# Optimization experiments

Hardware: AMD Instinct MI355X
Metric: run time of the kernel (lower is better)

## Reference

```python
import jax, jax.numpy as jnp
import numpy as np

N = 10000   # num_nodes
E = 320000  # num_edges (avg degree 32)
IN, HID, OUT = 512, 512, 256


def setup_inputs() -> dict:
    key = jax.random.key(0)
    ks = jax.random.split(key, 19)
    rn = lambda k, shape: (jax.random.normal(k, shape, jnp.float32) * 0.05)
    edge_index = jax.random.randint(ks[0], (2, E), 0, N, dtype=jnp.int32)
    return {
        "edge_index": edge_index,
        "w_pe": rn(ks[1], (IN, N)), "b_pe": rn(ks[2], (IN,)),
        "w_self0": rn(ks[3], (HID, IN)), "w_neigh0": rn(ks[4], (HID, IN)), "b0": rn(ks[5], (HID,)),
        "w_res0": rn(ks[6], (HID, IN)), "rb0": rn(ks[7], (HID,)),
        "w_self1": rn(ks[8], (HID, HID)), "w_neigh1": rn(ks[9], (HID, HID)), "b1": rn(ks[10], (HID,)),
        "w_res1": rn(ks[11], (HID, HID)), "rb1": rn(ks[12], (HID,)),
        "w_self2": rn(ks[13], (OUT, HID)), "w_neigh2": rn(ks[14], (OUT, HID)), "b2": rn(ks[15], (OUT,)),
        "w_res2": rn(ks[16], (OUT, HID)), "rb2": rn(ks[17], (OUT,)),
    }


def reference(edge_index, w_pe, b_pe,
              w_self0, w_neigh0, b0, w_res0, rb0,
              w_self1, w_neigh1, b1, w_res1, rb1,
              w_self2, w_neigh2, b2, w_res2, rb2):
    src, dst = edge_index[0], edge_index[1]

    def mean_agg(h):
        # mean of neighbor features per destination node (sparse SAGE aggregation)
        s = jax.ops.segment_sum(h[src], dst, num_segments=N)           # [N, D]
        deg = jax.ops.segment_sum(jnp.ones((E,), h.dtype), dst, num_segments=N)
        return s / jnp.maximum(deg, 1.0)[:, None]

    # pe = Linear(eye(N)) as in the original module
    pe = jnp.eye(N, dtype=w_pe.dtype) @ w_pe.T + b_pe                   # [N, IN]

    layers = [
        (w_self0, w_neigh0, b0, w_res0, rb0),
        (w_self1, w_neigh1, b1, w_res1, rb1),
        (w_self2, w_neigh2, b2, w_res2, rb2),
    ]

    h = pe
    mids = []
    for i, (ws, wn, b, wr, rb) in enumerate(layers):
        h_prev = h
        # SAGEConv (mean): fc_self(h) + fc_neigh(mean_neigh(h))
        h = h @ ws.T + mean_agg(h_prev) @ wn.T + b
        if i != len(layers) - 1:
            h = jax.nn.leaky_relu(h, 0.01)
            # F.dropout with training=False is identity (inference reference)
        h = h + (h_prev @ wr.T + rb)  # residual linear
        mids.append(h)
    return (h, *mids)
```

## Files before the change

### kernel.cpp

```cpp
#include <hip/hip_runtime.h>

#define N_NODES 10000
#define N_EDGES 320000
#define DIN 512
#define DHID 512
#define DOUT 256

typedef __bf16 bf16x8 __attribute__((ext_vector_type(8)));
typedef float f32x4 __attribute__((ext_vector_type(4)));
typedef unsigned short ushort_t;
typedef unsigned int uint_t;

__device__ __forceinline__ float b2f(ushort_t u){
    union { uint_t i; float f; } v; v.i = (uint_t)u << 16; return v.f;
}
__device__ __forceinline__ float blo(uint_t v){
    union { uint_t i; float f; } u; u.i = v << 16; return u.f;
}
__device__ __forceinline__ float bhi(uint_t v){
    union { uint_t i; float f; } u; u.i = v & 0xffff0000u; return u.f;
}
__device__ __forceinline__ ushort_t f2b(float f){
    union { float f; uint_t i; } v; v.f = f;
    uint_t i = v.i;
    return (ushort_t)((i + 0x7fffu + ((i >> 16) & 1u)) >> 16);
}

__device__ __forceinline__ void gll16(const ushort_t* g, ushort_t* l){
    __builtin_amdgcn_global_load_lds(
        (const __attribute__((address_space(1))) unsigned int*)g,
        (__attribute__((address_space(3))) unsigned int*)l,
        16, 0, 0);
}


__global__ void k_zero(int* __restrict__ deg, uint_t* __restrict__ zp){
    int i = blockIdx.x * 256 + threadIdx.x;
    if (i < N_NODES) deg[i] = 0;
    if (i < 256) zp[i] = 0u;
}

__global__ void k_degree(const int* __restrict__ dst, int* __restrict__ deg){
    int e = blockIdx.x * 256 + threadIdx.x;
    if (e < N_EDGES) atomicAdd(&deg[dst[e]], 1);
}

__global__ void k_scan(const int* __restrict__ deg, int* __restrict__ row_ptr,
                       int* __restrict__ cursor){
    __shared__ int part[256];
    int t = threadIdx.x;
    int base = t * 40;
    int loc[40];
    int s = 0;
    #pragma unroll
    for (int i = 0; i < 40; ++i){
        int idx = base + i;
        int v = (idx < N_NODES) ? deg[idx] : 0;
        s += v; loc[i] = s;
    }
    part[t] = s;
    __syncthreads();
    int val = s;
    for (int off = 1; off < 256; off <<= 1){
        int x = (t >= off) ? part[t - off] : 0;
        __syncthreads();
        val += x; part[t] = val;
        __syncthreads();
    }
    int exc = val - s;
    if (t == 0) row_ptr[0] = 0;
    int run = exc;
    #pragma unroll
    for (int i = 0; i < 40; ++i){
        int idx = base + i;
        if (idx < N_NODES){
            row_ptr[idx + 1] = exc + loc[i];
            cursor[idx] = run;
        }
        run = exc + loc[i];
    }
}

__global__ void k_scatter(const int* __restrict__ src, const int* __restrict__ dst,
                          int* __restrict__ cursor, int* __restrict__ srcs){
    int e = blockIdx.x * 256 + threadIdx.x;
    if (e < N_EDGES){
        int p = atomicAdd(&cursor[dst[e]], 1);
        srcs[p] = src[e];
    }
}


struct CvtArgs { const float* s[8]; const float* s2[8]; ushort_t* d[8]; int n[8]; };

__global__ void k_cvt(CvtArgs a){
    int m = blockIdx.y;
    int i = (blockIdx.x * 256 + threadIdx.x) * 8;
    if (i < a.n[m]){
        const float* sp = a.s[m] + i;
        float4 f0 = *(const float4*)sp;
        float4 f1 = *(const float4*)(sp + 4);
        if (a.s2[m]){
            const float* sq = a.s2[m] + i;
            float4 g0 = *(const float4*)sq;
            float4 g1 = *(const float4*)(sq + 4);
            f0.x += g0.x; f0.y += g0.y; f0.z += g0.z; f0.w += g0.w;
            f1.x += g1.x; f1.y += g1.y; f1.z += g1.z; f1.w += g1.w;
        }
        uint4 u;
        u.x = (uint_t)f2b(f0.x) | ((uint_t)f2b(f0.y) << 16);
        u.y = (uint_t)f2b(f0.z) | ((uint_t)f2b(f0.w) << 16);
        u.z = (uint_t)f2b(f1.x) | ((uint_t)f2b(f1.y) << 16);
        u.w = (uint_t)f2b(f1.z) | ((uint_t)f2b(f1.w) << 16);
        *(uint4*)&a.d[m][i] = u;
    }
}


__global__ void k_pe(const float* __restrict__ w_pe, const float* __restrict__ b_pe,
                     ushort_t* __restrict__ h0){
    __shared__ float lt[64][68];
    int t = threadIdx.x;
    int n0 = blockIdx.x * 64, i0 = blockIdx.y * 64;
    int nc = (t & 15) * 4, ir = t >> 4;
    #pragma unroll
    for (int p = 0; p < 4; ++p){
        int i_loc = ir + p * 16;
        float4 v = {0.f, 0.f, 0.f, 0.f};
        if (n0 + nc < N_NODES)
            v = *(const float4*)&w_pe[(size_t)(i0 + i_loc) * N_NODES + n0 + nc];
        lt[nc + 0][i_loc] = v.x;
        lt[nc + 1][i_loc] = v.y;
        lt[nc + 2][i_loc] = v.z;
        lt[nc + 3][i_loc] = v.w;
    }
    __syncthreads();
    int ic = t & 7, nr = t >> 3;
    #pragma unroll
    for (int p = 0; p < 2; ++p){
        int n_loc = nr + p * 32;
        int n = n0 + n_loc;
        if (n < N_NODES){
            uint4 u;
            uint_t w01 = (uint_t)f2b(lt[n_loc][ic*8+0] + b_pe[i0+ic*8+0])
                       | ((uint_t)f2b(lt[n_loc][ic*8+1] + b_pe[i0+ic*8+1]) << 16);
            uint_t w23 = (uint_t)f2b(lt[n_loc][ic*8+2] + b_pe[i0+ic*8+2])
                       | ((uint_t)f2b(lt[n_loc][ic*8+3] + b_pe[i0+ic*8+3]) << 16);
            uint_t w45 = (uint_t)f2b(lt[n_loc][ic*8+4] + b_pe[i0+ic*8+4])
                       | ((uint_t)f2b(lt[n_loc][ic*8+5] + b_pe[i0+ic*8+5]) << 16);
            uint_t w67 = (uint_t)f2b(lt[n_loc][ic*8+6] + b_pe[i0+ic*8+6])
                       | ((uint_t)f2b(lt[n_loc][ic*8+7] + b_pe[i0+ic*8+7]) << 16);
            u.x = w01; u.y = w23; u.z = w45; u.w = w67;
            *(uint4*)&h0[(size_t)n * DIN + i0 + ic * 8] = u;
        }
    }
}


#define AGG_EDGE(e, CH) { \
    int s_ = __builtin_amdgcn_readlane(sr, (e)); \
    uint_t v_ = *(const uint_t*)&X[((size_t)(uint_t)s_ << 9) + col]; \
    CH##0 += blo(v_); CH##1 += bhi(v_); }

__global__ __launch_bounds__(256) void k_agg(
    const ushort_t* __restrict__ X, const int* __restrict__ row_ptr,
    const int* __restrict__ srcs, ushort_t* __restrict__ out, int dummy)
{
    int w = threadIdx.x >> 6, lane = threadIdx.x & 63;
    int n = blockIdx.x * 4 + w;
    int col = blockIdx.y * 128 + lane * 2;
    int beg = row_ptr[n], end = row_ptr[n + 1];
    int deg = end - beg;
    float a0=0.f,a1=0.f, p0=0.f,p1=0.f, c0=0.f,c1=0.f, d0=0.f,d1=0.f;

    for (int base = beg; base < end; base += 64){
        int rem = end - base;
        int sr = (lane < rem) ? srcs[base + lane] : dummy;
        int cnt = rem < 64 ? rem : 64;
        #pragma unroll
        for (int k = 0; k < 4; ++k){
            if (k * 16 < cnt){
                int L = k * 16;
                AGG_EDGE(L + 0,  a) AGG_EDGE(L + 1,  p) AGG_EDGE(L + 2,  c) AGG_EDGE(L + 3,  d)
                AGG_EDGE(L + 4,  a) AGG_EDGE(L + 5,  p) AGG_EDGE(L + 6,  c) AGG_EDGE(L + 7,  d)
                AGG_EDGE(L + 8,  a) AGG_EDGE(L + 9,  p) AGG_EDGE(L + 10, c) AGG_EDGE(L + 11, d)
                AGG_EDGE(L + 12, a) AGG_EDGE(L + 13, p) AGG_EDGE(L + 14, c) AGG_EDGE(L + 15, d)
            }
        }
    }

    float r0 = (a0 + p0) + (c0 + d0);
    float r1 = (a1 + p1) + (c1 + d1);
    float inv = (deg > 0) ? 1.f / (float)deg : 1.f;
    uint_t o = (uint_t)f2b(r0 * inv) | ((uint_t)f2b(r1 * inv) << 16);
    *(uint_t*)&out[(size_t)n * 512 + col] = o;
}


#define AGGF_EDGE(e, CH) { \
    int s_ = __builtin_amdgcn_readlane(sr, (e)); \
    uint_t v_ = *(const uint_t*)&P[((size_t)(uint_t)s_ << 8) + col]; \
    CH##0 += blo(v_); CH##1 += bhi(v_); }

__global__ __launch_bounds__(256) void k_aggf(
    const ushort_t* __restrict__ P, const int* __restrict__ row_ptr,
    const int* __restrict__ srcs, const float* __restrict__ Q,
    float* __restrict__ fin, float* __restrict__ mid2, int dummy)
{
    int w = threadIdx.x >> 6, lane = threadIdx.x & 63;
    int n = blockIdx.x * 4 + w;
    int col = blockIdx.y * 128 + lane * 2;
    int beg = row_ptr[n], end = row_ptr[n + 1];
    int deg = end - beg;
    float a0=0.f,a1=0.f, p0=0.f,p1=0.f, c0=0.f,c1=0.f, d0=0.f,d1=0.f;

    for (int base = beg; base < end; base += 64){
        int rem = end - base;
        int sr = (lane < rem) ? srcs[base + lane] : dummy;
        int cnt = rem < 64 ? rem : 64;
        #pragma unroll
        for (int k = 0; k < 4; ++k){
            if (k * 16 < cnt){
                int L = k * 16;
                AGGF_EDGE(L + 0,  a) AGGF_EDGE(L + 1,  p) AGGF_EDGE(L + 2,  c) AGGF_EDGE(L + 3,  d)
                AGGF_EDGE(L + 4,  a) AGGF_EDGE(L + 5,  p) AGGF_EDGE(L + 6,  c) AGGF_EDGE(L + 7,  d)
                AGGF_EDGE(L + 8,  a) AGGF_EDGE(L + 9,  p) AGGF_EDGE(L + 10, c) AGGF_EDGE(L + 11, d)
                AGGF_EDGE(L + 12, a) AGGF_EDGE(L + 13, p) AGGF_EDGE(L + 14, c) AGGF_EDGE(L + 15, d)
            }
        }
    }

    float r0 = (a0 + p0) + (c0 + d0);
    float r1 = (a1 + p1) + (c1 + d1);
    float inv = (deg > 0) ? 1.f / (float)deg : 1.f;
    float2 q = *(const float2*)&Q[(size_t)n * 256 + col];
    float2 o;
    o.x = q.x + r0 * inv;
    o.y = q.y + r1 * inv;
    *(float2*)&fin [(size_t)n * 256 + col] = o;
    *(float2*)&mid2[(size_t)n * 256 + col] = o;
}


template<int DO, int BN, bool ACT, bool WRITE_BF>
__global__ __launch_bounds__(256, 2) void k_layer(
    const ushort_t* __restrict__ X, const ushort_t* __restrict__ G,
    const ushort_t* __restrict__ Ws, const ushort_t* __restrict__ Wn,
    const ushort_t* __restrict__ Wr,
    const float* __restrict__ b, const float* __restrict__ rb,
    float* __restrict__ Y, ushort_t* __restrict__ YB)
{
    constexpr int BM   = 160;
    constexpr int NT   = DO / BN;
    constexpr int WTN  = BN / 32;
    constexpr int NCH  = (2 * BM + 3 * BN) / 16;
    constexpr int CHPW = (NCH + 3) / 4;
    constexpr int OG   = BM * 32;
    constexpr int OS   = 2 * BM * 32;
    constexpr int WS32 = BN * 32;
    constexpr int BUFSZ = OS + 3 * WS32;
    __shared__ __align__(16) ushort_t smem[2][BUFSZ];

    int t = threadIdx.x;
    int bid = blockIdx.x;
    int r8 = bid & 7, q8 = bid >> 3;
    int m_t = (q8 / NT) * 8 + r8;
    int n_t = q8 % NT;
    if (m_t * BM >= N_NODES) return;
    int m0 = m_t * BM, n0 = n_t * BN;

    int lane = t & 63, w = t >> 6;
    int wr = w >> 1, wc = w & 1;

    const ushort_t* gptr[CHPW];
    int coff[CHPW];
    bool gv[CHPW];
    int rl = lane >> 2, sl = (lane & 3) * 8;
    #pragma unroll
    for (int i = 0; i < CHPW; ++i){
        int qq = w * CHPW + i;
        gv[i] = (qq < NCH);
        int qc = gv[i] ? qq : 0;
        const ushort_t* gA; int rowbase, off;
        if (qc < 10)      { gA = X;  rowbase = m0 + qc * 16;        off = qc * 512; }
        else if (qc < 20) { gA = G;  rowbase = m0 + (qc - 10) * 16; off = OG + (qc - 10) * 512; }
        else {
            int q2 = qc - 20;
            int sec = q2 / (BN / 16), wi = q2 % (BN / 16);
            gA = (sec == 0) ? Ws : (sec == 1) ? Wn : Wr;
            rowbase = n0 + wi * 16;
            off = OS + sec * WS32 + wi * 512;
        }
        gptr[i] = gA + (size_t)(rowbase + rl) * 512 + sl;
        coff[i] = off;
    }

    f32x4 accS[5][WTN] = {}, accG[5][WTN] = {}, accR[5][WTN] = {};
    int r16 = lane & 15;
    int arow = wr * 80 + r16;
    int brow = wc * (BN / 2) + r16;
    int kk = (lane >> 4) * 8;

    #pragma unroll
    for (int i = 0; i < CHPW; ++i) if (gv[i]) gll16(gptr[i], &smem[0][coff[i]]);
    __syncthreads();

    int cur = 0;
    for (int ks = 0; ks < 16; ++ks){
        if (ks < 15){
            int k0 = (ks + 1) * 32;
            #pragma unroll
            for (int i = 0; i < CHPW; ++i) if (gv[i]) gll16(gptr[i] + k0, &smem[cur ^ 1][coff[i]]);
        }

        const ushort_t* sb = smem[cur];
        bf16x8 ax[5], ag[5], bs[WTN], bn_[WTN], brr[WTN];
        #pragma unroll
        for (int m = 0; m < 5; ++m){
            ax[m] = *(const bf16x8*)&sb[(arow + m * 16) * 32 + kk];
            ag[m] = *(const bf16x8*)&sb[OG + (arow + m * 16) * 32 + kk];
        }
        #pragma unroll
        for (int n = 0; n < WTN; ++n){
            bs[n]  = *(const bf16x8*)&sb[OS            + (brow + n * 16) * 32 + kk];
            bn_[n] = *(const bf16x8*)&sb[OS + WS32     + (brow + n * 16) * 32 + kk];
            brr[n] = *(const bf16x8*)&sb[OS + 2 * WS32 + (brow + n * 16) * 32 + kk];
        }
        #pragma unroll
        for (int m = 0; m < 5; ++m)
            #pragma unroll
            for (int n = 0; n < WTN; ++n){
                accS[m][n] = __builtin_amdgcn_mfma_f32_16x16x32_bf16(ax[m], bs[n],  accS[m][n], 0, 0, 0);
                accG[m][n] = __builtin_amdgcn_mfma_f32_16x16x32_bf16(ag[m], bn_[n], accG[m][n], 0, 0, 0);
                accR[m][n] = __builtin_amdgcn_mfma_f32_16x16x32_bf16(ax[m], brr[n], accR[m][n], 0, 0, 0);
            }

        __syncthreads();
        cur ^= 1;
    }

    int col_l = lane & 15;
    int row_l = (lane >> 4) * 4;
    #pragma unroll
    for (int n = 0; n < WTN; ++n){
        int col = n0 + wc * (BN / 2) + n * 16 + col_l;
        float bb = b[col], rbb = rb[col];
        #pragma unroll
        for (int m = 0; m < 5; ++m){
            #pragma unroll
            for (int j = 0; j < 4; ++j){
                int row = m0 + wr * 80 + m * 16 + row_l + j;
                if (row < N_NODES){
                    float v = accS[m][n][j] + accG[m][n][j] + bb;
                    if (ACT) v = (v > 0.f) ? v : 0.01f * v;
                    v += accR[m][n][j] + rbb;
                    Y[(size_t)row * DO + col] = v;
                    if (WRITE_BF) YB[(size_t)row * DO + col] = f2b(v);
                }
            }
        }
    }
}


__global__ __launch_bounds__(256, 2) void k_layer2(
    const ushort_t* __restrict__ X,
    const ushort_t* __restrict__ Wn, const ushort_t* __restrict__ Wsr,
    const float* __restrict__ b, const float* __restrict__ rb,
    ushort_t* __restrict__ Pout, float* __restrict__ Qout)
{
    constexpr int BM = 160, BN = 32, NT = DOUT / BN;
    constexpr int NCH = 10 + 2 * (BN / 16);
    constexpr int CHPW = 4;
    constexpr int OWN = BM * 32;
    constexpr int OWS = OWN + BN * 32;
    constexpr int BUFSZ = OWS + BN * 32;
    __shared__ __align__(16) ushort_t smem[2][BUFSZ];

    int t = threadIdx.x;
    int bid = blockIdx.x;
    int r8 = bid & 7, q8 = bid >> 3;
    int m_t = (q8 / NT) * 8 + r8;
    int n_t = q8 % NT;
    if (m_t * BM >= N_NODES) return;
    int m0 = m_t * BM, n0 = n_t * BN;

    int lane = t & 63, w = t >> 6;
    int wr = w >> 1, wc = w & 1;

    const ushort_t* gptr[CHPW];
    int coff[CHPW];
    bool gv[CHPW];
    int rl = lane >> 2, sl = (lane & 3) * 8;
    #pragma unroll
    for (int i = 0; i < CHPW; ++i){
        int qq = w * CHPW + i;
        gv[i] = (qq < NCH);
        int qc = gv[i] ? qq : 0;
        const ushort_t* gA; int rowbase, off;
        if (qc < 10)      { gA = X;   rowbase = m0 + qc * 16;        off = qc * 512; }
        else if (qc < 12) { gA = Wn;  rowbase = n0 + (qc - 10) * 16; off = OWN + (qc - 10) * 512; }
        else              { gA = Wsr; rowbase = n0 + (qc - 12) * 16; off = OWS + (qc - 12) * 512; }
        gptr[i] = gA + (size_t)(rowbase + rl) * 512 + sl;
        coff[i] = off;
    }

    f32x4 accP[5] = {}, accQ[5] = {};
    int r16 = lane & 15;
    int arow = wr * 80 + r16;
    int brow = wc * 16 + r16;
    int kk = (lane >> 4) * 8;

    #pragma unroll
    for (int i = 0; i < CHPW; ++i) if (gv[i]) gll16(gptr[i], &smem[0][coff[i]]);
    __syncthreads();

    int cur = 0;
    for (int ks = 0; ks < 16; ++ks){
        if (ks < 15){
            int k0 = (ks + 1) * 32;
            #pragma unroll
            for (int i = 0; i < CHPW; ++i) if (gv[i]) gll16(gptr[i] + k0, &smem[cur ^ 1][coff[i]]);
        }

        const ushort_t* sb = smem[cur];
        bf16x8 ax[5];
        #pragma unroll
        for (int m = 0; m < 5; ++m)
            ax[m] = *(const bf16x8*)&sb[(arow + m * 16) * 32 + kk];
        bf16x8 bn_ = *(const bf16x8*)&sb[OWN + brow * 32 + kk];
        bf16x8 bsr = *(const bf16x8*)&sb[OWS + brow * 32 + kk];
        #pragma unroll
        for (int m = 0; m < 5; ++m){
            accP[m] = __builtin_amdgcn_mfma_f32_16x16x32_bf16(ax[m], bn_, accP[m], 0, 0, 0);
            accQ[m] = __builtin_amdgcn_mfma_f32_16x16x32_bf16(ax[m], bsr, accQ[m], 0, 0, 0);
        }

        __syncthreads();
        cur ^= 1;
    }

    int col_l = lane & 15;
    int row_l = (lane >> 4) * 4;
    int col = n0 + wc * 16 + col_l;
    float bb = b[col] + rb[col];
    #pragma unroll
    for (int m = 0; m < 5; ++m){
        #pragma unroll
        for (int j = 0; j < 4; ++j){
            int row = m0 + wr * 80 + m * 16 + row_l + j;
            if (row < N_NODES){
                Qout[(size_t)row * DOUT + col] = accQ[m][j] + bb;
                Pout[(size_t)row * DOUT + col] = f2b(accP[m][j]);
            }
        }
    }
}


extern "C" void kernel_launch(void* const* d_in, const int* in_sizes, int n_in,
                              void* d_out, int out_size, void* d_ws, size_t ws_size,
                              hipStream_t stream) {
    const int* edge  = (const int*)d_in[0];
    const int* e_src = edge;
    const int* e_dst = edge + N_EDGES;
    const float* w_pe = (const float*)d_in[1];
    const float* b_pe = (const float*)d_in[2];
    const float* ws0 = (const float*)d_in[3];
    const float* wn0 = (const float*)d_in[4];
    const float* b0  = (const float*)d_in[5];
    const float* wr0 = (const float*)d_in[6];
    const float* rb0 = (const float*)d_in[7];
    const float* ws1 = (const float*)d_in[8];
    const float* wn1 = (const float*)d_in[9];
    const float* b1  = (const float*)d_in[10];
    const float* wr1 = (const float*)d_in[11];
    const float* rb1 = (const float*)d_in[12];
    const float* ws2 = (const float*)d_in[13];
    const float* wn2 = (const float*)d_in[14];
    const float* b2  = (const float*)d_in[15];
    const float* wr2 = (const float*)d_in[16];
    const float* rb2 = (const float*)d_in[17];

    char* wsb = (char*)d_ws;
    ushort_t* h0   = (ushort_t*)wsb;
    ushort_t* hb   = (ushort_t*)(wsb + 10240000);
    ushort_t* aggb = (ushort_t*)(wsb + 20480000);
    ushort_t* wbf  = (ushort_t*)(wsb + 30720000);
    int* deg     = (int*)(wsb + 34652160);
    int* row_ptr = deg + 10016;
    int* cursor  = row_ptr + 10016;
    int* srcs    = cursor + 10016;
    uint_t* zp   = (uint_t*)(wsb + 36052992);
    const int dummy_h0 = 35208;
    const int dummy_hb = 25208;
    const int dummy_pb = 30416;

    ushort_t* wbf0s = wbf;
    ushort_t* wbf0n = wbf + 262144;
    ushort_t* wbf0r = wbf + 524288;
    ushort_t* wbf1s = wbf + 786432;
    ushort_t* wbf1n = wbf + 1048576;
    ushort_t* wbf1r = wbf + 1310720;
    ushort_t* wbf2n = wbf + 1572864;
    ushort_t* wbf2sr= wbf + 1703936;

    float* out  = (float*)d_out;
    float* fin  = out;
    float* mid0 = out + 2560000;
    float* mid1 = out + 7680000;
    float* mid2 = out + 12800000;
    ushort_t* pb = aggb;

    k_zero   <<<40, 256, 0, stream>>>(deg, zp);
    k_degree <<<1250, 256, 0, stream>>>(e_dst, deg);
    k_scan   <<<1, 256, 0, stream>>>(deg, row_ptr, cursor);
    k_scatter<<<1250, 256, 0, stream>>>(e_src, e_dst, cursor, srcs);

    CvtArgs ca;
    ca.s[0]=ws0; ca.s[1]=wn0; ca.s[2]=wr0;
    ca.s[3]=ws1; ca.s[4]=wn1; ca.s[5]=wr1;
    ca.s[6]=wn2; ca.s[7]=ws2;
    for (int i = 0; i < 8; ++i) ca.s2[i] = nullptr;
    ca.s2[7] = wr2;
    ca.d[0]=wbf0s; ca.d[1]=wbf0n; ca.d[2]=wbf0r;
    ca.d[3]=wbf1s; ca.d[4]=wbf1n; ca.d[5]=wbf1r;
    ca.d[6]=wbf2n; ca.d[7]=wbf2sr;
    for (int i = 0; i < 6; ++i) ca.n[i] = 262144;
    ca.n[6] = 131072; ca.n[7] = 131072;
    k_cvt<<<dim3(128, 8), 256, 0, stream>>>(ca);

    k_pe<<<dim3(157, 8), 256, 0, stream>>>(w_pe, b_pe, h0);

    k_agg<<<dim3(2500, 4), 256, 0, stream>>>(h0, row_ptr, srcs, aggb, dummy_h0);
    k_layer<512, 64, true, true ><<<dim3(512), 256, 0, stream>>>(
        h0, aggb, wbf0s, wbf0n, wbf0r, b0, rb0, mid0, hb);

    k_agg<<<dim3(2500, 4), 256, 0, stream>>>(hb, row_ptr, srcs, aggb, dummy_hb);
    k_layer<512, 64, true, true ><<<dim3(512), 256, 0, stream>>>(
        hb, aggb, wbf1s, wbf1n, wbf1r, b1, rb1, mid1, h0);

    k_layer2<<<dim3(512), 256, 0, stream>>>(h0, wbf2n, wbf2sr, b2, rb2, pb, mid2);
    k_aggf<<<dim3(2500, 2), 256, 0, stream>>>(pb, row_ptr, srcs, mid2, fin, mid2, dummy_pb);
}
```

Baseline: 214.1 us.

## Merge prologue kernels and process two nodes per wave in aggregation

Folds the weight conversion, positional-embedding transpose and degree zeroing into one launch, cutting three kernel launches. The aggregation kernels now assign each half-wave to its own destination node and have each lane load 8-byte uint2 chunks, halving the grid and doubling the bytes per load. The two halves of a wave loop to the larger of their two degrees, so some work is wasted when neighbouring nodes' degrees differ.

```diff
diff --git a/kernel.cpp b/kernel.cpp
--- a/kernel.cpp
+++ b/kernel.cpp
@@ -33,12 +33,6 @@
         16, 0, 0);
 }
 
-
-__global__ void k_zero(int* __restrict__ deg, uint_t* __restrict__ zp){
-    int i = blockIdx.x * 256 + threadIdx.x;
-    if (i < N_NODES) deg[i] = 0;
-    if (i < 256) zp[i] = 0u;
-}
 
 __global__ void k_degree(const int* __restrict__ dst, int* __restrict__ deg){
     int e = blockIdx.x * 256 + threadIdx.x;
@@ -93,114 +87,127 @@
 
 struct CvtArgs { const float* s[8]; const float* s2[8]; ushort_t* d[8]; int n[8]; };
 
-__global__ void k_cvt(CvtArgs a){
-    int m = blockIdx.y;
-    int i = (blockIdx.x * 256 + threadIdx.x) * 8;
-    if (i < a.n[m]){
-        const float* sp = a.s[m] + i;
-        float4 f0 = *(const float4*)sp;
-        float4 f1 = *(const float4*)(sp + 4);
-        if (a.s2[m]){
-            const float* sq = a.s2[m] + i;
-            float4 g0 = *(const float4*)sq;
-            float4 g1 = *(const float4*)(sq + 4);
-            f0.x += g0.x; f0.y += g0.y; f0.z += g0.z; f0.w += g0.w;
-            f1.x += g1.x; f1.y += g1.y; f1.z += g1.z; f1.w += g1.w;
-        }
-        uint4 u;
-        u.x = (uint_t)f2b(f0.x) | ((uint_t)f2b(f0.y) << 16);
-        u.y = (uint_t)f2b(f0.z) | ((uint_t)f2b(f0.w) << 16);
-        u.z = (uint_t)f2b(f1.x) | ((uint_t)f2b(f1.y) << 16);
-        u.w = (uint_t)f2b(f1.z) | ((uint_t)f2b(f1.w) << 16);
-        *(uint4*)&a.d[m][i] = u;
-    }
-}
-
-
-__global__ void k_pe(const float* __restrict__ w_pe, const float* __restrict__ b_pe,
-                     ushort_t* __restrict__ h0){
+__global__ void k_pro(const float* __restrict__ w_pe, const float* __restrict__ b_pe,
+                      ushort_t* __restrict__ h0, CvtArgs a,
+                      int* __restrict__ deg, uint_t* __restrict__ zp){
     __shared__ float lt[64][68];
+    int bid = blockIdx.x;
     int t = threadIdx.x;
-    int n0 = blockIdx.x * 64, i0 = blockIdx.y * 64;
-    int nc = (t & 15) * 4, ir = t >> 4;
-    #pragma unroll
-    for (int p = 0; p < 4; ++p){
-        int i_loc = ir + p * 16;
-        float4 v = {0.f, 0.f, 0.f, 0.f};
-        if (n0 + nc < N_NODES)
-            v = *(const float4*)&w_pe[(size_t)(i0 + i_loc) * N_NODES + n0 + nc];
-        lt[nc + 0][i_loc] = v.x;
-        lt[nc + 1][i_loc] = v.y;
-        lt[nc + 2][i_loc] = v.z;
-        lt[nc + 3][i_loc] = v.w;
-    }
-    __syncthreads();
-    int ic = t & 7, nr = t >> 3;
-    #pragma unroll
-    for (int p = 0; p < 2; ++p){
-        int n_loc = nr + p * 32;
-        int n = n0 + n_loc;
-        if (n < N_NODES){
+    if (bid < 1256){
+        int n0 = (bid % 157) * 64, i0 = (bid / 157) * 64;
+        int nc = (t & 15) * 4, ir = t >> 4;
+        #pragma unroll
+        for (int p = 0; p < 4; ++p){
+            int i_loc = ir + p * 16;
+            float4 v = {0.f, 0.f, 0.f, 0.f};
+            if (n0 + nc < N_NODES)
+                v = *(const float4*)&w_pe[(size_t)(i0 + i_loc) * N_NODES + n0 + nc];
+            lt[nc + 0][i_loc] = v.x;
+            lt[nc + 1][i_loc] = v.y;
+            lt[nc + 2][i_loc] = v.z;
+            lt[nc + 3][i_loc] = v.w;
+        }
+        __syncthreads();
+        int ic = t & 7, nr = t >> 3;
+        #pragma unroll
+        for (int p = 0; p < 2; ++p){
+            int n_loc = nr + p * 32;
+            int n = n0 + n_loc;
+            if (n < N_NODES){
+                uint4 u;
+                u.x = (uint_t)f2b(lt[n_loc][ic*8+0] + b_pe[i0+ic*8+0])
+                    | ((uint_t)f2b(lt[n_loc][ic*8+1] + b_pe[i0+ic*8+1]) << 16);
+                u.y = (uint_t)f2b(lt[n_loc][ic*8+2] + b_pe[i0+ic*8+2])
+                    | ((uint_t)f2b(lt[n_loc][ic*8+3] + b_pe[i0+ic*8+3]) << 16);
+                u.z = (uint_t)f2b(lt[n_loc][ic*8+4] + b_pe[i0+ic*8+4])
+                    | ((uint_t)f2b(lt[n_loc][ic*8+5] + b_pe[i0+ic*8+5]) << 16);
+                u.w = (uint_t)f2b(lt[n_loc][ic*8+6] + b_pe[i0+ic*8+6])
+                    | ((uint_t)f2b(lt[n_loc][ic*8+7] + b_pe[i0+ic*8+7]) << 16);
+                *(uint4*)&h0[(size_t)n * DIN + i0 + ic * 8] = u;
+            }
+        }
+    } else if (bid < 2280){
+        int j = bid - 1256;
+        int m = j >> 7;
+        int i = (((j & 127) * 256) + t) * 8;
+        if (i < a.n[m]){
+            const float* sp = a.s[m] + i;
+            float4 f0 = *(const float4*)sp;
+            float4 f1 = *(const float4*)(sp + 4);
+            if (a.s2[m]){
+                const float* sq = a.s2[m] + i;
+                float4 g0 = *(const float4*)sq;
+                float4 g1 = *(const float4*)(sq + 4);
+                f0.x += g0.x; f0.y += g0.y; f0.z += g0.z; f0.w += g0.w;
+                f1.x += g1.x; f1.y += g1.y; f1.z += g1.z; f1.w += g1.w;
+            }
             uint4 u;
-            uint_t w01 = (uint_t)f2b(lt[n_loc][ic*8+0] + b_pe[i0+ic*8+0])
-                       | ((uint_t)f2b(lt[n_loc][ic*8+1] + b_pe[i0+ic*8+1]) << 16);
-            uint_t w23 = (uint_t)f2b(lt[n_loc][ic*8+2] + b_pe[i0+ic*8+2])
-                       | ((uint_t)f2b(lt[n_loc][ic*8+3] + b_pe[i0+ic*8+3]) << 16);
-            uint_t w45 = (uint_t)f2b(lt[n_loc][ic*8+4] + b_pe[i0+ic*8+4])
-                       | ((uint_t)f2b(lt[n_loc][ic*8+5] + b_pe[i0+ic*8+5]) << 16);
-            uint_t w67 = (uint_t)f2b(lt[n_loc][ic*8+6] + b_pe[i0+ic*8+6])
-                       | ((uint_t)f2b(lt[n_loc][ic*8+7] + b_pe[i0+ic*8+7]) << 16);
-            u.x = w01; u.y = w23; u.z = w45; u.w = w67;
-            *(uint4*)&h0[(size_t)n * DIN + i0 + ic * 8] = u;
-        }
-    }
-}
-
-
-#define AGG_EDGE(e, CH) { \
-    int s_ = __builtin_amdgcn_readlane(sr, (e)); \
-    uint_t v_ = *(const uint_t*)&X[((size_t)(uint_t)s_ << 9) + col]; \
-    CH##0 += blo(v_); CH##1 += bhi(v_); }
+            u.x = (uint_t)f2b(f0.x) | ((uint_t)f2b(f0.y) << 16);
+            u.y = (uint_t)f2b(f0.z) | ((uint_t)f2b(f0.w) << 16);
+            u.z = (uint_t)f2b(f1.x) | ((uint_t)f2b(f1.y) << 16);
+            u.w = (uint_t)f2b(f1.z) | ((uint_t)f2b(f1.w) << 16);
+            *(uint4*)&a.d[m][i] = u;
+        }
+    } else {
+        int i = (bid - 2280) * 256 + t;
+        if (i < N_NODES) deg[i] = 0;
+        if (i < 256) zp[i] = 0u;
+    }
+}
+
+
+#define DUAL_EDGE(X, SH, e, CH) { \
+    int rA_ = __builtin_amdgcn_readlane(sr, (e)); \
+    int rB_ = __builtin_amdgcn_readlane(sr, 32 + (e)); \
+    int row_ = half ? rB_ : rA_; \
+    uint2 v_ = *(const uint2*)&X[((size_t)(uint_t)row_ << SH) + col]; \
+    CH##0 += blo(v_.x); CH##1 += bhi(v_.x); CH##2 += blo(v_.y); CH##3 += bhi(v_.y); }
 
 __global__ __launch_bounds__(256) void k_agg(
     const ushort_t* __restrict__ X, const int* __restrict__ row_ptr,
     const int* __restrict__ srcs, ushort_t* __restrict__ out, int dummy)
 {
     int w = threadIdx.x >> 6, lane = threadIdx.x & 63;
-    int n = blockIdx.x * 4 + w;
-    int col = blockIdx.y * 128 + lane * 2;
+    int half = lane >> 5, l32 = lane & 31;
+    int n = blockIdx.x * 8 + w * 2 + half;
+    int col = blockIdx.y * 128 + l32 * 4;
     int beg = row_ptr[n], end = row_ptr[n + 1];
     int deg = end - beg;
-    float a0=0.f,a1=0.f, p0=0.f,p1=0.f, c0=0.f,c1=0.f, d0=0.f,d1=0.f;
-
-    for (int base = beg; base < end; base += 64){
-        int rem = end - base;
-        int sr = (lane < rem) ? srcs[base + lane] : dummy;
-        int cnt = rem < 64 ? rem : 64;
-        #pragma unroll
-        for (int k = 0; k < 4; ++k){
+    int degMax = max(deg, __shfl_xor(deg, 32));
+    float a0=0.f,a1=0.f,a2=0.f,a3=0.f, b0=0.f,b1=0.f,b2=0.f,b3=0.f;
+    float c0=0.f,c1=0.f,c2=0.f,c3=0.f, d0=0.f,d1=0.f,d2=0.f,d3=0.f;
+
+    for (int base = 0; base < degMax; base += 32){
+        int rem = deg - base;
+        int sr = (l32 < rem) ? srcs[beg + base + l32] : dummy;
+        int cnt = degMax - base; if (cnt > 32) cnt = 32;
+        #pragma unroll
+        for (int k = 0; k < 2; ++k){
             if (k * 16 < cnt){
                 int L = k * 16;
-                AGG_EDGE(L + 0,  a) AGG_EDGE(L + 1,  p) AGG_EDGE(L + 2,  c) AGG_EDGE(L + 3,  d)
-                AGG_EDGE(L + 4,  a) AGG_EDGE(L + 5,  p) AGG_EDGE(L + 6,  c) AGG_EDGE(L + 7,  d)
-                AGG_EDGE(L + 8,  a) AGG_EDGE(L + 9,  p) AGG_EDGE(L + 10, c) AGG_EDGE(L + 11, d)
-                AGG_EDGE(L + 12, a) AGG_EDGE(L + 13, p) AGG_EDGE(L + 14, c) AGG_EDGE(L + 15, d)
-            }
-        }
-    }
-
-    float r0 = (a0 + p0) + (c0 + d0);
-    float r1 = (a1 + p1) + (c1 + d1);
+                DUAL_EDGE(X, 9, L + 0,  a) DUAL_EDGE(X, 9, L + 1,  b)
+                DUAL_EDGE(X, 9, L + 2,  c) DUAL_EDGE(X, 9, L + 3,  d)
+                DUAL_EDGE(X, 9, L + 4,  a) DUAL_EDGE(X, 9, L + 5,  b)
+                DUAL_EDGE(X, 9, L + 6,  c) DUAL_EDGE(X, 9, L + 7,  d)
+                DUAL_EDGE(X, 9, L + 8,  a) DUAL_EDGE(X, 9, L + 9,  b)
+                DUAL_EDGE(X, 9, L + 10, c) DUAL_EDGE(X, 9, L + 11, d)
+                DUAL_EDGE(X, 9, L + 12, a) DUAL_EDGE(X, 9, L + 13, b)
+                DUAL_EDGE(X, 9, L + 14, c) DUAL_EDGE(X, 9, L + 15, d)
+            }
+        }
+    }
+
+    float r0 = (a0 + b0) + (c0 + d0);
+    float r1 = (a1 + b1) + (c1 + d1);
+    float r2 = (a2 + b2) + (c2 + d2);
+    float r3 = (a3 + b3) + (c3 + d3);
     float inv = (deg > 0) ? 1.f / (float)deg : 1.f;
-    uint_t o = (uint_t)f2b(r0 * inv) | ((uint_t)f2b(r1 * inv) << 16);
-    *(uint_t*)&out[(size_t)n * 512 + col] = o;
-}
-
-
-#define AGGF_EDGE(e, CH) { \
-    int s_ = __builtin_amdgcn_readlane(sr, (e)); \
-    uint_t v_ = *(const uint_t*)&P[((size_t)(uint_t)s_ << 8) + col]; \
-    CH##0 += blo(v_); CH##1 += bhi(v_); }
+    uint2 o;
+    o.x = (uint_t)f2b(r0 * inv) | ((uint_t)f2b(r1 * inv) << 16);
+    o.y = (uint_t)f2b(r2 * inv) | ((uint_t)f2b(r3 * inv) << 16);
+    *(uint2*)&out[(size_t)n * 512 + col] = o;
+}
+
 
 __global__ __launch_bounds__(256) void k_aggf(
     const ushort_t* __restrict__ P, const int* __restrict__ row_ptr,
@@ -208,37 +215,48 @@
     float* __restrict__ fin, float* __restrict__ mid2, int dummy)
 {
     int w = threadIdx.x >> 6, lane = threadIdx.x & 63;
-    int n = blockIdx.x * 4 + w;
-    int col = blockIdx.y * 128 + lane * 2;
+    int half = lane >> 5, l32 = lane & 31;
+    int n = blockIdx.x * 8 + w * 2 + half;
+    int col = blockIdx.y * 128 + l32 * 4;
     int beg = row_ptr[n], end = row_ptr[n + 1];
     int deg = end - beg;
-    float a0=0.f,a1=0.f, p0=0.f,p1=0.f, c0=0.f,c1=0.f, d0=0.f,d1=0.f;
-
-    for (int base = beg; base < end; base += 64){
-        int rem = end - base;
-        int sr = (lane < rem) ? srcs[base + lane] : dummy;
-        int cnt = rem < 64 ? rem : 64;
-        #pragma unroll
-        for (int k = 0; k < 4; ++k){
+    int degMax = max(deg, __shfl_xor(deg, 32));
+    float a0=0.f,a1=0.f,a2=0.f,a3=0.f, b0=0.f,b1=0.f,b2=0.f,b3=0.f;
+    float c0=0.f,c1=0.f,c2=0.f,c3=0.f, d0=0.f,d1=0.f,d2=0.f,d3=0.f;
+
+    for (int base = 0; base < degMax; base += 32){
+        int rem = deg - base;
+        int sr = (l32 < rem) ? srcs[beg + base + l32] : dummy;
+        int cnt = degMax - base; if (cnt > 32) cnt = 32;
+        #pragma unroll
+        for (int k = 0; k < 2; ++k){
             if (k * 16 < cnt){
                 int L = k * 16;
-                AGGF_EDGE(L + 0,  a) AGGF_EDGE(L + 1,  p) AGGF_EDGE(L + 2,  c) AGGF_EDGE(L + 3,  d)
-                AGGF_EDGE(L + 4,  a) AGGF_EDGE(L + 5,  p) AGGF_EDGE(L + 6,  c) AGGF_EDGE(L + 7,  d)
-                AGGF_EDGE(L + 8,  a) AGGF_EDGE(L + 9,  p) AGGF_EDGE(L + 10, c) AGGF_EDGE(L + 11, d)
-                AGGF_EDGE(L + 12, a) AGGF_EDGE(L + 13, p) AGGF_EDGE(L + 14, c) AGGF_EDGE(L + 15, d)
-            }
-        }
-    }
-
-    float r0 = (a0 + p0) + (c0 + d0);
-    float r1 = (a1 + p1) + (c1 + d1);
+                DUAL_EDGE(P, 8, L + 0,  a) DUAL_EDGE(P, 8, L + 1,  b)
+                DUAL_EDGE(P, 8, L + 2,  c) DUAL_EDGE(P, 8, L + 3,  d)
+                DUAL_EDGE(P, 8, L + 4,  a) DUAL_EDGE(P, 8, L + 5,  b)
+                DUAL_EDGE(P, 8, L + 6,  c) DUAL_EDGE(P, 8, L + 7,  d)
+                DUAL_EDGE(P, 8, L + 8,  a) DUAL_EDGE(P, 8, L + 9,  b)
+                DUAL_EDGE(P, 8, L + 10, c) DUAL_EDGE(P, 8, L + 11, d)
+                DUAL_EDGE(P, 8, L + 12, a) DUAL_EDGE(P, 8, L + 13, b)
+                DUAL_EDGE(P, 8, L + 14, c) DUAL_EDGE(P, 8, L + 15, d)
+            }
+        }
+    }
+
+    float r0 = (a0 + b0) + (c0 + d0);
+    float r1 = (a1 + b1) + (c1 + d1);
+    float r2 = (a2 + b2) + (c2 + d2);
+    float r3 = (a3 + b3) + (c3 + d3);
     float inv = (deg > 0) ? 1.f / (float)deg : 1.f;
-    float2 q = *(const float2*)&Q[(size_t)n * 256 + col];
-    float2 o;
+    float4 q = *(const float4*)&Q[(size_t)n * 256 + col];
+    float4 o;
     o.x = q.x + r0 * inv;
     o.y = q.y + r1 * inv;
-    *(float2*)&fin [(size_t)n * 256 + col] = o;
-    *(float2*)&mid2[(size_t)n * 256 + col] = o;
+    o.z = q.z + r2 * inv;
+    o.w = q.w + r3 * inv;
+    *(float4*)&fin [(size_t)n * 256 + col] = o;
+    *(float4*)&mid2[(size_t)n * 256 + col] = o;
 }
 
 
@@ -512,11 +530,6 @@
     float* mid2 = out + 12800000;
     ushort_t* pb = aggb;
 
-    k_zero   <<<40, 256, 0, stream>>>(deg, zp);
-    k_degree <<<1250, 256, 0, stream>>>(e_dst, deg);
-    k_scan   <<<1, 256, 0, stream>>>(deg, row_ptr, cursor);
-    k_scatter<<<1250, 256, 0, stream>>>(e_src, e_dst, cursor, srcs);
-
     CvtArgs ca;
     ca.s[0]=ws0; ca.s[1]=wn0; ca.s[2]=wr0;
     ca.s[3]=ws1; ca.s[4]=wn1; ca.s[5]=wr1;
@@ -528,18 +541,21 @@
     ca.d[6]=wbf2n; ca.d[7]=wbf2sr;
     for (int i = 0; i < 6; ++i) ca.n[i] = 262144;
     ca.n[6] = 131072; ca.n[7] = 131072;
-    k_cvt<<<dim3(128, 8), 256, 0, stream>>>(ca);
-
-    k_pe<<<dim3(157, 8), 256, 0, stream>>>(w_pe, b_pe, h0);
-
-    k_agg<<<dim3(2500, 4), 256, 0, stream>>>(h0, row_ptr, srcs, aggb, dummy_h0);
+
+    k_pro<<<2320, 256, 0, stream>>>(w_pe, b_pe, h0, ca, deg, zp);
+
+    k_degree <<<1250, 256, 0, stream>>>(e_dst, deg);
+    k_scan   <<<1, 256, 0, stream>>>(deg, row_ptr, cursor);
+    k_scatter<<<1250, 256, 0, stream>>>(e_src, e_dst, cursor, srcs);
+
+    k_agg<<<dim3(1250, 4), 256, 0, stream>>>(h0, row_ptr, srcs, aggb, dummy_h0);
     k_layer<512, 64, true, true ><<<dim3(512), 256, 0, stream>>>(
         h0, aggb, wbf0s, wbf0n, wbf0r, b0, rb0, mid0, hb);
 
-    k_agg<<<dim3(2500, 4), 256, 0, stream>>>(hb, row_ptr, srcs, aggb, dummy_hb);
+    k_agg<<<dim3(1250, 4), 256, 0, stream>>>(hb, row_ptr, srcs, aggb, dummy_hb);
     k_layer<512, 64, true, true ><<<dim3(512), 256, 0, stream>>>(
         hb, aggb, wbf1s, wbf1n, wbf1r, b1, rb1, mid1, h0);
 
     k_layer2<<<dim3(512), 256, 0, stream>>>(h0, wbf2n, wbf2sr, b2, rb2, pb, mid2);
-    k_aggf<<<dim3(2500, 2), 256, 0, stream>>>(pb, row_ptr, srcs, mid2, fin, mid2, dummy_pb);
-}
+    k_aggf<<<dim3(1250, 2), 256, 0, stream>>>(pb, row_ptr, srcs, mid2, fin, mid2, dummy_pb);
+}
```

After: 221.2 us. +3.3%, slower.
